# Performance work log

Measured on AMD Instinct MI355X. Metric: run time of the kernel, lower is better.

## Reference

```python
import jax, jax.numpy as jnp
import numpy as np

N_NODES = 100000
N_EDGES = 1200000
D = 64
N_REL = 2
N_BASIS = 16
N_LAYERS = 3  # num_layer=2 -> 3 stacked CompGCNLayer stages


def setup_inputs() -> dict:
    key = jax.random.key(0)
    ks = jax.random.split(key, 12)
    s = 1.0 / np.sqrt(D)
    return {
        "h_u": jax.random.normal(ks[0], (N_NODES, D), jnp.float32),
        "Basis": jax.random.normal(ks[1], (N_BASIS, D), jnp.float32) * (1.0 / np.sqrt(N_BASIS)),
        "alpha": jax.random.normal(ks[2], (N_REL + 1, N_BASIS), jnp.float32),
        "W_O": jax.random.normal(ks[3], (N_LAYERS, D, D), jnp.float32) * s,
        "W_I": jax.random.normal(ks[4], (N_LAYERS, D, D), jnp.float32) * s,
        "W_S": jax.random.normal(ks[5], (N_LAYERS, D, D), jnp.float32) * s,
        "W_rel": jax.random.normal(ks[6], (N_LAYERS, D, D), jnp.float32) * s,
        "src": jax.random.randint(ks[7], (N_EDGES,), 0, N_NODES, jnp.int32),
        "dst": jax.random.randint(ks[8], (N_EDGES,), 0, N_NODES, jnp.int32),
        "edge_etype": jax.random.randint(ks[9], (N_EDGES,), 0, N_REL, jnp.int32),
        "edge_dir": jax.random.randint(ks[10], (N_EDGES,), 0, 2, jnp.int32),  # 0=out, 1=in
    }


def reference(h_u, Basis, alpha, W_O, W_I, W_S, W_rel, src, dst, edge_etype, edge_dir):
    # relation representations: rows 0..N_REL-1 are etypes, row N_REL is self_loop
    h_r = alpha @ Basis  # [N_REL+1, D]
    is_in = (edge_dir == 1)[:, None]  # [E,1]

    for l in range(N_LAYERS):
        # composition 'sub': comp_m = h_src - h_edge_rel
        comp_m = h_u[src] - h_r[edge_etype]               # [E, D]
        # per-direction linear transform (Linear: x @ W.T)
        m_out = comp_m @ W_O[l].T
        m_in = comp_m @ W_I[l].T
        msg = jnp.where(is_in, m_in, m_out)               # [E, D]
        # scatter-sum aggregation (copy_e + sum)
        agg = jax.ops.segment_sum(msg, dst, num_segments=N_NODES)  # [N, D]
        # self-loop branch
        comp_s = h_u - h_r[-1]                            # [N, D]
        h_v = comp_s @ W_S[l].T + agg
        h_r = h_r @ W_rel[l].T
        if l < N_LAYERS - 1:  # last layer has act=None
            h_v = jax.nn.relu(h_v)
            h_r = jax.nn.relu(h_r)
        h_u = h_v
    return h_u
```

## Files before the change

kernel.cpp:

```cpp
#include <hip/hip_runtime.h>

constexpr int D = 64;
constexpr int NBASIS = 16;
constexpr int NLAYERS = 3;
constexpr int SCAN_CHUNK = 1024;
constexpr int BSH = 9;
constexpr int BNODES = 1 << BSH;
constexpr int PB = 256;
constexpr int NR = 128;

__global__ void hr_all_kernel(const float* __restrict__ alpha,
                              const float* __restrict__ basis,
                              const float* __restrict__ Wrel,
                              float* __restrict__ hr) {
  __shared__ float cur[192], nxt[192];
  int t = threadIdx.x;
  int r = t >> 6, d = t & 63;
  float s = 0.f;
  for (int b = 0; b < NBASIS; ++b) s += alpha[r * NBASIS + b] * basis[b * D + d];
  cur[t] = s;
  hr[t] = s;
  __syncthreads();
  for (int l = 0; l < NLAYERS - 1; ++l) {
    float v = 0.f;
    for (int k = 0; k < D; ++k) v += cur[r * D + k] * Wrel[l * D * D + d * D + k];
    v = fmaxf(v, 0.f);
    nxt[t] = v;
    hr[(l + 1) * 192 + t] = v;
    __syncthreads();
    cur[t] = nxt[t];
    __syncthreads();
  }
}

__global__ __launch_bounds__(256) void part_hist(const int* __restrict__ dst,
                                                 int* __restrict__ ghist,
                                                 int E, int chunk, int NB) {
  __shared__ int lh[512];
  int blk = blockIdx.x, t = threadIdx.x;
  for (int i = t; i < NB; i += 256) lh[i] = 0;
  __syncthreads();
  int beg = blk * chunk;
  int end = beg + chunk < E ? beg + chunk : E;
  for (int j = beg + t; j < end; j += 256) atomicAdd(&lh[dst[j] >> BSH], 1);
  __syncthreads();
  for (int i = t; i < NB; i += 256) ghist[(size_t)i * PB + blk] = lh[i];
}

__global__ void scan_partial(const int* __restrict__ cnt, int* __restrict__ bsums, int M) {
  int t = threadIdx.x;
  int base = blockIdx.x * SCAN_CHUNK + t * 4;
  int s = 0;
  if (base + 3 < M) {
    int4 v = *(const int4*)(cnt + base);
    s = v.x + v.y + v.z + v.w;
  } else {
    for (int i = 0; i < 4; ++i) if (base + i < M) s += cnt[base + i];
  }
  for (int off = 32; off > 0; off >>= 1) s += __shfl_down(s, off, 64);
  __shared__ int ws[4];
  if ((t & 63) == 0) ws[t >> 6] = s;
  __syncthreads();
  if (t == 0) bsums[blockIdx.x] = ws[0] + ws[1] + ws[2] + ws[3];
}

__global__ void scan_bsums(const int* __restrict__ bsums, int* __restrict__ boffs,
                           int SB, int* __restrict__ totalp) {
  __shared__ int sh[128];
  int t = threadIdx.x;
  int v = (t < SB) ? bsums[t] : 0;
  sh[t] = v;
  __syncthreads();
  for (int off = 1; off < 128; off <<= 1) {
    int u = (t >= off) ? sh[t - off] : 0;
    __syncthreads();
    sh[t] += u;
    __syncthreads();
  }
  if (t < SB) boffs[t] = sh[t] - v;
  if (t == SB - 1) *totalp = sh[t];
}

__global__ void scan_final(const int* __restrict__ cnt, const int* __restrict__ boffs,
                           int* __restrict__ out, int M) {
  int t = threadIdx.x;
  int base = blockIdx.x * SCAN_CHUNK + t * 4;
  int v0 = 0, v1 = 0, v2 = 0, v3 = 0;
  if (base + 3 < M) {
    int4 v = *(const int4*)(cnt + base);
    v0 = v.x; v1 = v.y; v2 = v.z; v3 = v.w;
  } else {
    if (base + 0 < M) v0 = cnt[base + 0];
    if (base + 1 < M) v1 = cnt[base + 1];
    if (base + 2 < M) v2 = cnt[base + 2];
    if (base + 3 < M) v3 = cnt[base + 3];
  }
  int ts = v0 + v1 + v2 + v3;
  int lane = t & 63;
  int incl = ts;
  for (int off = 1; off < 64; off <<= 1) {
    int u = __shfl_up(incl, off, 64);
    if (lane >= off) incl += u;
  }
  __shared__ int wsum[4];
  if (lane == 63) wsum[t >> 6] = incl;
  __syncthreads();
  int woff = 0;
  for (int w = 0; w < (t >> 6); ++w) woff += wsum[w];
  int run = boffs[blockIdx.x] + woff + incl - ts;
  if (base + 0 < M) out[base + 0] = run;
  if (base + 1 < M) out[base + 1] = run + v0;
  if (base + 2 < M) out[base + 2] = run + v0 + v1;
  if (base + 3 < M) out[base + 3] = run + v0 + v1 + v2;
}

__global__ __launch_bounds__(256) void part_scatter(
    const int* __restrict__ src, const int* __restrict__ dst,
    const int* __restrict__ et, const int* __restrict__ dir,
    const int* __restrict__ goffs, int* __restrict__ tmp,
    int E, int chunk, int NB) {
  __shared__ int lc[512];
  int blk = blockIdx.x, t = threadIdx.x;
  for (int i = t; i < NB; i += 256) lc[i] = goffs[(size_t)i * PB + blk];
  __syncthreads();
  int beg = blk * chunk;
  int end = beg + chunk < E ? beg + chunk : E;
  for (int j = beg + t; j < end; j += 256) {
    int d = dst[j];
    int b = d >> BSH;
    int p = atomicAdd(&lc[b], 1);
    tmp[p] = src[j] | (et[j] << 17) | (dir[j] << 18) | ((d & (BNODES - 1)) << 19);
  }
}

__global__ __launch_bounds__(256) void bucket_finalize(
    const int* __restrict__ tmp, const int* __restrict__ goffs,
    int* __restrict__ startv, int* __restrict__ perm, int N, int NB, int E) {
  __shared__ int lcnt[BNODES];
  __shared__ int lcur[BNODES];
  __shared__ int spair[256];
  int b = blockIdx.x, t = threadIdx.x;
  int beg = goffs[(size_t)b * PB];
  int end = (b == NB - 1) ? E : goffs[(size_t)(b + 1) * PB];
  lcnt[t] = 0;
  lcnt[t + 256] = 0;
  __syncthreads();
  for (int j = beg + t; j < end; j += 256)
    atomicAdd(&lcnt[(tmp[j] >> 19) & (BNODES - 1)], 1);
  __syncthreads();
  int c0 = lcnt[2 * t], c1 = lcnt[2 * t + 1];
  spair[t] = c0 + c1;
  __syncthreads();
  for (int off = 1; off < 256; off <<= 1) {
    int u = (t >= off) ? spair[t - off] : 0;
    __syncthreads();
    spair[t] += u;
    __syncthreads();
  }
  int epair = spair[t] - (c0 + c1);
  lcur[2 * t] = epair;
  lcur[2 * t + 1] = epair + c0;
  int v0 = (b << BSH) + 2 * t;
  if (v0 < N) startv[v0] = beg + epair;
  if (v0 + 1 < N) startv[v0 + 1] = beg + epair + c0;
  if (b == NB - 1 && t == 0) startv[N] = E;
  __syncthreads();
  for (int j = beg + t; j < end; j += 256) {
    int w = tmp[j];
    int p = atomicAdd(&lcur[(w >> 19) & (BNODES - 1)], 1);
    perm[beg + p] = w & 0x7FFFF;
  }
}

__global__ __launch_bounds__(256) void gather_kernel(
    const float* __restrict__ h, const float* __restrict__ hr,
    const int* __restrict__ start, const int* __restrict__ perm,
    float* __restrict__ aggO, float* __restrict__ aggI, int N) {
  int lane = threadIdx.x & 63;
  int v = blockIdx.x * 4 + (threadIdx.x >> 6);
  if (v >= N) return;
  float hr0 = hr[lane];
  float hr1 = hr[D + lane];
  int beg = start[v], end = start[v + 1];
  float accO = 0.f, accI = 0.f;
  for (int j = beg; j < end; j += 8) {
    int pp[8];
    float ff[8];
#pragma unroll
    for (int u = 0; u < 8; ++u) {
      int jj = j + u < end ? j + u : beg;
      pp[u] = perm[jj];
    }
#pragma unroll
    for (int u = 0; u < 8; ++u)
      ff[u] = h[(size_t)(pp[u] & 0x1FFFF) * D + lane];
#pragma unroll
    for (int u = 0; u < 8; ++u) {
      if (j + u < end) {
        float c = ff[u] - (((pp[u] >> 17) & 1) ? hr1 : hr0);
        if (pp[u] & (1 << 18)) accI += c; else accO += c;
      }
    }
  }
  aggO[(size_t)v * D + lane] = accO;
  aggI[(size_t)v * D + lane] = accI;
}

__global__ __launch_bounds__(512) void node_gemm(
    const float* __restrict__ h_in, const float* __restrict__ aggO,
    const float* __restrict__ aggI, const float* __restrict__ WS,
    const float* __restrict__ WO, const float* __restrict__ WI,
    const float* __restrict__ hr_self, float* __restrict__ h_out,
    int do_relu, int N) {
  __shared__ float xh[NR][65], xo[NR][65], xi[NR][65];
  __shared__ float ws_[64][65], wo_[64][65], wi_[64][65];
  int tid = threadIdx.x;
  int row0 = blockIdx.x * NR;
  for (int idx = tid; idx < 1024; idx += 512) {
    int d = idx >> 4, k0 = (idx & 15) * 4;
    float4 a = ((const float4*)WS)[idx];
    float4 b = ((const float4*)WO)[idx];
    float4 c = ((const float4*)WI)[idx];
    ws_[d][k0] = a.x; ws_[d][k0+1] = a.y; ws_[d][k0+2] = a.z; ws_[d][k0+3] = a.w;
    wo_[d][k0] = b.x; wo_[d][k0+1] = b.y; wo_[d][k0+2] = b.z; wo_[d][k0+3] = b.w;
    wi_[d][k0] = c.x; wi_[d][k0+1] = c.y; wi_[d][k0+2] = c.z; wi_[d][k0+3] = c.w;
  }
  const float4* hr4 = (const float4*)hr_self;
  for (int idx = tid; idx < NR * 16; idx += 512) {
    int r = idx >> 4, kq = idx & 15, k0 = kq * 4;
    int row = row0 + r;
    float4 a = make_float4(0.f, 0.f, 0.f, 0.f), b = a, c = a;
    if (row < N) {
      size_t g = (size_t)row * 16 + kq;
      a = ((const float4*)h_in)[g];
      float4 hs = hr4[kq];
      a.x -= hs.x; a.y -= hs.y; a.z -= hs.z; a.w -= hs.w;
      b = ((const float4*)aggO)[g];
      c = ((const float4*)aggI)[g];
    }
    xh[r][k0] = a.x; xh[r][k0+1] = a.y; xh[r][k0+2] = a.z; xh[r][k0+3] = a.w;
    xo[r][k0] = b.x; xo[r][k0+1] = b.y; xo[r][k0+2] = b.z; xo[r][k0+3] = b.w;
    xi[r][k0] = c.x; xi[r][k0+1] = c.y; xi[r][k0+2] = c.z; xi[r][k0+3] = c.w;
  }
  __syncthreads();
  int tc4 = (tid & 15) * 4;
  int tr4 = (tid >> 4) * 4;
  float acc[4][4] = {{0.f}};
#define GEMM1(X, W)                                                          \
  _Pragma("unroll 4")                                                        \
  for (int k = 0; k < 64; ++k) {                                             \
    float x0 = X[tr4+0][k], x1 = X[tr4+1][k], x2 = X[tr4+2][k], x3 = X[tr4+3][k]; \
    float w0 = W[tc4+0][k], w1 = W[tc4+1][k], w2 = W[tc4+2][k], w3 = W[tc4+3][k]; \
    acc[0][0]+=x0*w0; acc[0][1]+=x0*w1; acc[0][2]+=x0*w2; acc[0][3]+=x0*w3;  \
    acc[1][0]+=x1*w0; acc[1][1]+=x1*w1; acc[1][2]+=x1*w2; acc[1][3]+=x1*w3;  \
    acc[2][0]+=x2*w0; acc[2][1]+=x2*w1; acc[2][2]+=x2*w2; acc[2][3]+=x2*w3;  \
    acc[3][0]+=x3*w0; acc[3][1]+=x3*w1; acc[3][2]+=x3*w2; acc[3][3]+=x3*w3;  \
  }
  GEMM1(xh, ws_)
  GEMM1(xo, wo_)
  GEMM1(xi, wi_)
#undef GEMM1
#pragma unroll
  for (int i = 0; i < 4; ++i) {
    int row = row0 + tr4 + i;
    if (row < N) {
      float4 o = make_float4(acc[i][0], acc[i][1], acc[i][2], acc[i][3]);
      if (do_relu) {
        o.x = fmaxf(o.x, 0.f); o.y = fmaxf(o.y, 0.f);
        o.z = fmaxf(o.z, 0.f); o.w = fmaxf(o.w, 0.f);
      }
      ((float4*)h_out)[(size_t)row * 16 + (tc4 >> 2)] = o;
    }
  }
}

extern "C" void kernel_launch(void* const* d_in, const int* in_sizes, int n_in,
                              void* d_out, int out_size, void* d_ws, size_t ws_size,
                              hipStream_t stream) {
  const float* h_u   = (const float*)d_in[0];
  const float* Basis = (const float*)d_in[1];
  const float* alpha = (const float*)d_in[2];
  const float* W_O   = (const float*)d_in[3];
  const float* W_I   = (const float*)d_in[4];
  const float* W_S   = (const float*)d_in[5];
  const float* W_rel = (const float*)d_in[6];
  const int* src  = (const int*)d_in[7];
  const int* dst  = (const int*)d_in[8];
  const int* et   = (const int*)d_in[9];
  const int* edir = (const int*)d_in[10];
  int N = in_sizes[0] / D;
  int E = in_sizes[7];
  int NB = (N + BNODES - 1) >> BSH;
  int M = NB * PB;
  int chunk = (E + PB - 1) / PB;

  char* ws = (char*)d_ws;
  size_t off = 0;
  auto alloc = [&](size_t bytes) -> void* {
    void* p = ws + off;
    off = (off + bytes + 255) & ~(size_t)255;
    return p;
  };
  float* h_buf = (float*)alloc((size_t)N * D * 4);
  float* aggO  = (float*)alloc((size_t)N * D * 4);
  float* aggI  = (float*)alloc((size_t)N * D * 4);
  float* hrbuf = (float*)alloc(3 * 192 * 4);
  int* startv  = (int*)alloc((size_t)(N + 1) * 4);
  int* perm    = (int*)alloc((size_t)E * 4);
  int* tmp     = (int*)alloc((size_t)E * 4);
  int* ghist   = (int*)alloc((size_t)M * 4);
  int* goffs   = (int*)alloc((size_t)(M + 1) * 4);
  int SB = (M + SCAN_CHUNK - 1) / SCAN_CHUNK;
  int* bsums   = (int*)alloc((size_t)SB * 4);
  int* boffs   = (int*)alloc((size_t)SB * 4);

  part_hist<<<PB, 256, 0, stream>>>(dst, ghist, E, chunk, NB);
  scan_partial<<<SB, 256, 0, stream>>>(ghist, bsums, M);
  scan_bsums<<<1, 128, 0, stream>>>(bsums, boffs, SB, goffs + M);
  scan_final<<<SB, 256, 0, stream>>>(ghist, boffs, goffs, M);
  part_scatter<<<PB, 256, 0, stream>>>(src, dst, et, edir, goffs, tmp, E, chunk, NB);
  bucket_finalize<<<NB, 256, 0, stream>>>(tmp, goffs, startv, perm, N, NB, E);

  hr_all_kernel<<<1, 192, 0, stream>>>(alpha, Basis, W_rel, hrbuf);

  int nb_g = (N + 3) / 4;
  int nb_n = (N + NR - 1) / NR;
  for (int l = 0; l < NLAYERS; ++l) {
    const float* h_src = (l == 0) ? h_u : h_buf;
    const float* hr_l = hrbuf + l * 192;
    gather_kernel<<<nb_g, 256, 0, stream>>>(h_src, hr_l, startv, perm, aggO, aggI, N);
    float* outp = (l == NLAYERS - 1) ? (float*)d_out : h_buf;
    node_gemm<<<nb_n, 512, 0, stream>>>(
        h_src, aggO, aggI,
        W_S + (size_t)l * D * D, W_O + (size_t)l * D * D, W_I + (size_t)l * D * D,
        hr_l + 2 * D, outp, (l < NLAYERS - 1) ? 1 : 0, N);
  }
}
```

Before: 567.4 us.

## Restructure node GEMM with transposed smem tiles and 8x4 register blocking

Rewrites the per-node GEMM to store X and W transposed in shared memory so the inner loop does float4 LDS reads, and gives each of 256 threads an 8x4 output tile instead of 4x4 with 512 threads. The three matrix products now run one after another through a single reused X/W buffer pair, which cuts shared memory from about 150KB to about 51KB and should allow more blocks per CU. The cost is extra barriers and serialized loads per product, and the transposed stores into smem may cause bank conflicts.

```diff
diff --git a/kernel.cpp b/kernel.cpp
--- a/kernel.cpp
+++ b/kernel.cpp
@@ -206,63 +206,72 @@
   aggI[(size_t)v * D + lane] = accI;
 }
 
-__global__ __launch_bounds__(512) void node_gemm(
+__global__ __launch_bounds__(256) void node_gemm(
     const float* __restrict__ h_in, const float* __restrict__ aggO,
     const float* __restrict__ aggI, const float* __restrict__ WS,
     const float* __restrict__ WO, const float* __restrict__ WI,
     const float* __restrict__ hr_self, float* __restrict__ h_out,
     int do_relu, int N) {
-  __shared__ float xh[NR][65], xo[NR][65], xi[NR][65];
-  __shared__ float ws_[64][65], wo_[64][65], wi_[64][65];
+  __shared__ float Xt[64][132];
+  __shared__ float Wt[64][68];
   int tid = threadIdx.x;
   int row0 = blockIdx.x * NR;
-  for (int idx = tid; idx < 1024; idx += 512) {
-    int d = idx >> 4, k0 = (idx & 15) * 4;
-    float4 a = ((const float4*)WS)[idx];
-    float4 b = ((const float4*)WO)[idx];
-    float4 c = ((const float4*)WI)[idx];
-    ws_[d][k0] = a.x; ws_[d][k0+1] = a.y; ws_[d][k0+2] = a.z; ws_[d][k0+3] = a.w;
-    wo_[d][k0] = b.x; wo_[d][k0+1] = b.y; wo_[d][k0+2] = b.z; wo_[d][k0+3] = b.w;
-    wi_[d][k0] = c.x; wi_[d][k0+1] = c.y; wi_[d][k0+2] = c.z; wi_[d][k0+3] = c.w;
-  }
+  int tr4 = (tid & 15) * 4;
+  int tc4 = (tid >> 4) * 4;
   const float4* hr4 = (const float4*)hr_self;
-  for (int idx = tid; idx < NR * 16; idx += 512) {
-    int r = idx >> 4, kq = idx & 15, k0 = kq * 4;
-    int row = row0 + r;
-    float4 a = make_float4(0.f, 0.f, 0.f, 0.f), b = a, c = a;
-    if (row < N) {
-      size_t g = (size_t)row * 16 + kq;
-      a = ((const float4*)h_in)[g];
-      float4 hs = hr4[kq];
-      a.x -= hs.x; a.y -= hs.y; a.z -= hs.z; a.w -= hs.w;
-      b = ((const float4*)aggO)[g];
-      c = ((const float4*)aggI)[g];
-    }
-    xh[r][k0] = a.x; xh[r][k0+1] = a.y; xh[r][k0+2] = a.z; xh[r][k0+3] = a.w;
-    xo[r][k0] = b.x; xo[r][k0+1] = b.y; xo[r][k0+2] = b.z; xo[r][k0+3] = b.w;
-    xi[r][k0] = c.x; xi[r][k0+1] = c.y; xi[r][k0+2] = c.z; xi[r][k0+3] = c.w;
-  }
-  __syncthreads();
-  int tc4 = (tid & 15) * 4;
-  int tr4 = (tid >> 4) * 4;
-  float acc[4][4] = {{0.f}};
-#define GEMM1(X, W)                                                          \
-  _Pragma("unroll 4")                                                        \
-  for (int k = 0; k < 64; ++k) {                                             \
-    float x0 = X[tr4+0][k], x1 = X[tr4+1][k], x2 = X[tr4+2][k], x3 = X[tr4+3][k]; \
-    float w0 = W[tc4+0][k], w1 = W[tc4+1][k], w2 = W[tc4+2][k], w3 = W[tc4+3][k]; \
-    acc[0][0]+=x0*w0; acc[0][1]+=x0*w1; acc[0][2]+=x0*w2; acc[0][3]+=x0*w3;  \
-    acc[1][0]+=x1*w0; acc[1][1]+=x1*w1; acc[1][2]+=x1*w2; acc[1][3]+=x1*w3;  \
-    acc[2][0]+=x2*w0; acc[2][1]+=x2*w1; acc[2][2]+=x2*w2; acc[2][3]+=x2*w3;  \
-    acc[3][0]+=x3*w0; acc[3][1]+=x3*w1; acc[3][2]+=x3*w2; acc[3][3]+=x3*w3;  \
-  }
-  GEMM1(xh, ws_)
-  GEMM1(xo, wo_)
-  GEMM1(xi, wi_)
-#undef GEMM1
-#pragma unroll
-  for (int i = 0; i < 4; ++i) {
-    int row = row0 + tr4 + i;
+  const float* xsrc[3] = {h_in, aggO, aggI};
+  const float* wsrc[3] = {WS, WO, WI};
+  float acc[8][4];
+#pragma unroll
+  for (int i = 0; i < 8; ++i)
+#pragma unroll
+    for (int j = 0; j < 4; ++j) acc[i][j] = 0.f;
+
+  for (int m = 0; m < 3; ++m) {
+    const float4* wp = (const float4*)wsrc[m];
+    for (int idx = tid; idx < 1024; idx += 256) {
+      int k4 = idx & 15, d = idx >> 4;
+      float4 w = wp[d * 16 + k4];
+      Wt[4 * k4 + 0][d] = w.x;
+      Wt[4 * k4 + 1][d] = w.y;
+      Wt[4 * k4 + 2][d] = w.z;
+      Wt[4 * k4 + 3][d] = w.w;
+    }
+    const float4* xp = (const float4*)xsrc[m];
+    for (int idx = tid; idx < 2048; idx += 256) {
+      int k4 = idx & 15, r = idx >> 4;
+      int row = row0 + r;
+      float4 a = make_float4(0.f, 0.f, 0.f, 0.f);
+      if (row < N) {
+        a = xp[(size_t)row * 16 + k4];
+        if (m == 0) {
+          float4 hs = hr4[k4];
+          a.x -= hs.x; a.y -= hs.y; a.z -= hs.z; a.w -= hs.w;
+        }
+      }
+      Xt[4 * k4 + 0][r] = a.x;
+      Xt[4 * k4 + 1][r] = a.y;
+      Xt[4 * k4 + 2][r] = a.z;
+      Xt[4 * k4 + 3][r] = a.w;
+    }
+    __syncthreads();
+#pragma unroll 2
+    for (int k = 0; k < 64; ++k) {
+      float4 xv0 = *(const float4*)&Xt[k][tr4];
+      float4 xv1 = *(const float4*)&Xt[k][tr4 + 64];
+      float4 wv  = *(const float4*)&Wt[k][tc4];
+      float xr[8] = {xv0.x, xv0.y, xv0.z, xv0.w, xv1.x, xv1.y, xv1.z, xv1.w};
+      float wr[4] = {wv.x, wv.y, wv.z, wv.w};
+#pragma unroll
+      for (int i = 0; i < 8; ++i)
+#pragma unroll
+        for (int j = 0; j < 4; ++j) acc[i][j] += xr[i] * wr[j];
+    }
+    __syncthreads();
+  }
+#pragma unroll
+  for (int i = 0; i < 8; ++i) {
+    int row = row0 + (i < 4 ? tr4 + i : 64 + tr4 + (i - 4));
     if (row < N) {
       float4 o = make_float4(acc[i][0], acc[i][1], acc[i][2], acc[i][3]);
       if (do_relu) {
@@ -330,7 +339,7 @@
     const float* hr_l = hrbuf + l * 192;
     gather_kernel<<<nb_g, 256, 0, stream>>>(h_src, hr_l, startv, perm, aggO, aggI, N);
     float* outp = (l == NLAYERS - 1) ? (float*)d_out : h_buf;
-    node_gemm<<<nb_n, 512, 0, stream>>>(
+    node_gemm<<<nb_n, 256, 0, stream>>>(
         h_src, aggO, aggI,
         W_S + (size_t)l * D * D, W_O + (size_t)l * D * D, W_I + (size_t)l * D * D,
         hr_l + 2 * D, outp, (l < NLAYERS - 1) ? 1 : 0, N);
```

Result: faster. 506.0 us (-10.8%).
